# Kernel tuning notes

Measured on AMD Instinct MI355X. Metric: run time of the kernel, lower is better.

The kernel has to match this reference:

```python
import jax, jax.numpy as jnp
import numpy as np

LEAK = 0.01
EPS = 1e-5


def _gcn(x, W, b, src, dst, n):
    # GCNConv: add self-loops, symmetric D^-1/2 (A+I) D^-1/2 normalization
    h = x @ W
    loop = jnp.arange(n)
    s = jnp.concatenate([src, loop])
    d = jnp.concatenate([dst, loop])
    deg = jax.ops.segment_sum(jnp.ones(s.shape[0], h.dtype), d, num_segments=n)
    dinv = jnp.where(deg > 0, jax.lax.rsqrt(deg), 0.0)
    norm = dinv[s] * dinv[d]
    out = jax.ops.segment_sum(h[s] * norm[:, None], d, num_segments=n)
    return out + b


def _sage(x, Wl, bl, Wr, src, dst, n):
    # SAGEConv (mean aggr): lin_l(mean_neigh) + lin_r(x); bias on lin_l
    cnt = jax.ops.segment_sum(jnp.ones(src.shape[0], x.dtype), dst, num_segments=n)
    agg = jax.ops.segment_sum(x[src], dst, num_segments=n) / jnp.maximum(cnt, 1.0)[:, None]
    return agg @ Wl + bl + x @ Wr


def _bn(x, g, b):
    # BatchNorm over node dim, batch statistics (training forward), biased var
    m = x.mean(0)
    v = jnp.mean((x - m) ** 2, axis=0)
    return (x - m) * jax.lax.rsqrt(v + EPS) * g + b


def _lrelu(x):
    return jnp.where(x >= 0, x, LEAK * x)


def setup_inputs() -> dict:
    key = jax.random.key(0)
    ks = jax.random.split(key, 20)
    N, E, F_IN, H, G, L = 50000, 800000, 128, 128, 1000, 1000
    h2, h4, OUT = H // 2, H // 4, 32
    x = jax.random.normal(ks[0], (N, F_IN), dtype=jnp.float32)
    edge_index = jax.random.randint(ks[1], (2, E), 0, N)
    batch = jnp.sort(jax.random.randint(ks[2], (N,), 0, G))
    link_indices = jax.random.randint(ks[3], (2, L), 0, G)
    s = 0.05
    return {
        "x": x, "edge_index": edge_index, "batch": batch,
        "link_indices": link_indices, "num_graphs": G,
        "W1": jax.random.normal(ks[4], (F_IN, H), jnp.float32) * s,
        "b1": jnp.zeros((H,), jnp.float32),
        "g1": jnp.ones((H,), jnp.float32), "be1": jnp.zeros((H,), jnp.float32),
        "Wl2": jax.random.normal(ks[5], (H, h2), jnp.float32) * s,
        "bl2": jnp.zeros((h2,), jnp.float32),
        "Wr2": jax.random.normal(ks[6], (H, h2), jnp.float32) * s,
        "g2": jnp.ones((h2,), jnp.float32), "be2": jnp.zeros((h2,), jnp.float32),
        "W3": jax.random.normal(ks[7], (h2, h4), jnp.float32) * s,
        "b3": jnp.zeros((h4,), jnp.float32),
        "g3": jnp.ones((h4,), jnp.float32), "be3": jnp.zeros((h4,), jnp.float32),
        "W4": jax.random.normal(ks[8], (h4, OUT), jnp.float32) * s,
        "b4": jnp.zeros((OUT,), jnp.float32),
    }


def reference(x, edge_index, batch, link_indices, num_graphs,
              W1, b1, g1, be1, Wl2, bl2, Wr2, g2, be2,
              W3, b3, g3, be3, W4, b4):
    n = x.shape[0]
    src, dst = edge_index[0], edge_index[1]
    h = _lrelu(_bn(_gcn(x, W1, b1, src, dst, n), g1, be1))        # dropout = identity (eval)
    h = _lrelu(_bn(_sage(h, Wl2, bl2, Wr2, src, dst, n), g2, be2))
    h = _lrelu(_bn(_gcn(h, W3, b3, src, dst, n), g3, be3))
    h = _gcn(h, W4, b4, src, dst, n)
    g = jax.ops.segment_sum(h, batch, num_segments=num_graphs)     # global_add_pool
    src_emb = g[link_indices[0]]
    tgt_emb = g[link_indices[1]]
    return jax.nn.sigmoid(jnp.sum(src_emb * tgt_emb, axis=1))
```

## Files before the change

kernel.cpp:

```cpp
#include <hip/hip_runtime.h>
#include <math.h>

#define LEAK 0.01f
#define BNEPS 1e-5f
#define NCH 256
#define NGMAX 1024

typedef __attribute__((ext_vector_type(8))) short bf16x8;
typedef __attribute__((ext_vector_type(4))) float f32x4;
typedef __attribute__((ext_vector_type(2))) float f32x2;

__device__ inline unsigned bfpack(float a, float b) {
  unsigned ua = __float_as_uint(a);
  unsigned ub = __float_as_uint(b);
  unsigned ra = (ua + 0x7fffu + ((ua >> 16) & 1u)) >> 16;
  unsigned rb = (ub + 0x7fffu + ((ub >> 16) & 1u)) & 0xffff0000u;
  return ra | rb;
}
__device__ inline unsigned short bfround(float a) {
  unsigned ua = __float_as_uint(a);
  return (unsigned short)((ua + 0x7fffu + ((ua >> 16) & 1u)) >> 16);
}
__device__ inline float2 bfunpack(unsigned u) {
  float2 r;
  r.x = __uint_as_float(u << 16);
  r.y = __uint_as_float(u & 0xffff0000u);
  return r;
}
__device__ inline unsigned char f32_to_fp8(float v) {
  int p = __builtin_amdgcn_cvt_pk_fp8_f32(v, v, 0, false);
  return (unsigned char)(p & 0xff);
}

__global__ __launch_bounds__(256) void k_hist(const int* __restrict__ dst,
                                              int* __restrict__ H, int E, int NBK) {
  __shared__ int h[256];
  h[threadIdx.x] = 0;
  __syncthreads();
  int chunk = (E + NCH - 1) / NCH;
  int lo = blockIdx.x * chunk, hi = min(lo + chunk, E);
  for (int e = lo + threadIdx.x; e < hi; e += 256)
    atomicAdd(&h[dst[e] >> 8], 1);
  __syncthreads();
  if (threadIdx.x < NBK) H[threadIdx.x * NCH + blockIdx.x] = h[threadIdx.x];
}

__global__ __launch_bounds__(256) void k_gscan1(const int* __restrict__ in,
                                                int* __restrict__ bsum, int m) {
  int i = blockIdx.x * 256 + threadIdx.x;
  int v = (i < m) ? in[i] : 0;
#pragma unroll
  for (int s = 1; s < 64; s <<= 1) v += __shfl_xor(v, s, 64);
  __shared__ int ws[4];
  if ((threadIdx.x & 63) == 0) ws[threadIdx.x >> 6] = v;
  __syncthreads();
  if (threadIdx.x == 0) bsum[blockIdx.x] = ws[0] + ws[1] + ws[2] + ws[3];
}
__global__ __launch_bounds__(256) void k_gscan2(int* __restrict__ bsum, int NB) {
  __shared__ int lds[256];
  int t = threadIdx.x;
  int v = (t < NB) ? bsum[t] : 0;
  lds[t] = v;
  __syncthreads();
  for (int ofs = 1; ofs < 256; ofs <<= 1) {
    int u = (t >= ofs) ? lds[t - ofs] : 0;
    __syncthreads();
    lds[t] += u;
    __syncthreads();
  }
  if (t < NB) bsum[t] = lds[t] - v;
}
__global__ __launch_bounds__(256) void k_gscan3(const int* __restrict__ in,
                                                const int* __restrict__ boff,
                                                int* __restrict__ out, int m) {
  __shared__ int lds[256];
  int t = threadIdx.x;
  int i = blockIdx.x * 256 + t;
  int v = (i < m) ? in[i] : 0;
  lds[t] = v;
  __syncthreads();
  for (int ofs = 1; ofs < 256; ofs <<= 1) {
    int u = (t >= ofs) ? lds[t - ofs] : 0;
    __syncthreads();
    lds[t] += u;
    __syncthreads();
  }
  if (i < m) out[i] = boff[blockIdx.x] + lds[t] - v;
}

__global__ __launch_bounds__(256) void k_scatter_bkt(
    const int* __restrict__ src, const int* __restrict__ dst,
    const int* __restrict__ O, int* __restrict__ ebuf, int E, int NBK) {
  __shared__ int cur[256];
  if (threadIdx.x < NBK) cur[threadIdx.x] = O[threadIdx.x * NCH + blockIdx.x];
  __syncthreads();
  int chunk = (E + NCH - 1) / NCH;
  int lo = blockIdx.x * chunk, hi = min(lo + chunk, E);
  for (int e = lo + threadIdx.x; e < hi; e += 256) {
    int d = dst[e];
    int pos = atomicAdd(&cur[d >> 8], 1);
    ebuf[pos] = src[e] | ((d & 255) << 24);
  }
}

__global__ __launch_bounds__(256) void k_fill2(
    const int* __restrict__ ebuf, const int* __restrict__ O,
    int* __restrict__ eidx, int* __restrict__ rowptr,
    float* __restrict__ dinv, float* __restrict__ invcnt,
    int E, int n, int NBK) {
  __shared__ int hist[256];
  __shared__ int sc[256];
  __shared__ int cur[256];
  const int b = blockIdx.x;
  const int t = threadIdx.x;
  const int lo = O[b * NCH];
  const int hi = (b + 1 < NBK) ? O[(b + 1) * NCH] : E;
  hist[t] = 0;
  __syncthreads();
  for (int e = lo + t; e < hi; e += 256)
    atomicAdd(&hist[(ebuf[e] >> 24) & 255], 1);
  __syncthreads();
  int v = hist[t];
  sc[t] = v;
  __syncthreads();
  for (int ofs = 1; ofs < 256; ofs <<= 1) {
    int u = (t >= ofs) ? sc[t - ofs] : 0;
    __syncthreads();
    sc[t] += u;
    __syncthreads();
  }
  int excl = sc[t] - v;
  cur[t] = lo + excl;
  int node = b * 256 + t;
  if (node < n) {
    rowptr[node] = lo + excl;
    float d = (float)v;
    dinv[node]   = rsqrtf(d + 1.0f);
    invcnt[node] = 1.0f / fmaxf(d, 1.0f);
  }
  if (node == n || (b == NBK - 1 && t == 255)) rowptr[n] = E;
  __syncthreads();
  for (int e = lo + t; e < hi; e += 256) {
    int p = ebuf[e];
    int pos = atomicAdd(&cur[(p >> 24) & 255], 1);
    eidx[pos] = p & 0xFFFFFF;
  }
}

template<int F, bool GCN, bool OUTBF, bool ADD>
__global__ __launch_bounds__(256) void k_gather(
    const unsigned short* __restrict__ Hs, const float* __restrict__ scale,
    const int* __restrict__ rowptr, const int* __restrict__ eidx,
    const float* __restrict__ bias, const float* __restrict__ addf,
    float* __restrict__ outf, unsigned short* __restrict__ outb, int n) {
  constexpr int COLS = F / 8;
  constexpr int EPI  = 64 / COLS;
  const int v = blockIdx.x * 4 + (threadIdx.x >> 6);
  if (v >= n) return;
  const int lane = threadIdx.x & 63;
  const int col  = lane % COLS;
  const int eo   = lane / COLS;

  const int lo = rowptr[v], hi = rowptr[v + 1];
  float a[8] = {0.f,0.f,0.f,0.f,0.f,0.f,0.f,0.f};
  int myE = (lo + lane < hi) ? eidx[lo + lane] : 0;
  for (int base = lo; base < hi; base += 64) {
    int cnt = min(hi - base, 64);
    int nxt = (base + 64 + lane < hi) ? eidx[base + 64 + lane] : 0;
#pragma unroll 4
    for (int t = eo; t < cnt; t += EPI) {
      int s = __shfl(myE, t, 64);
      uint4 hv = *(const uint4*)&Hs[(long long)s * F + col * 8];
      float2 p0 = bfunpack(hv.x), p1 = bfunpack(hv.y);
      float2 p2 = bfunpack(hv.z), p3 = bfunpack(hv.w);
      a[0]+=p0.x; a[1]+=p0.y; a[2]+=p1.x; a[3]+=p1.y;
      a[4]+=p2.x; a[5]+=p2.y; a[6]+=p3.x; a[7]+=p3.y;
    }
    myE = nxt;
  }
#pragma unroll
  for (int m = COLS; m < 64; m <<= 1) {
#pragma unroll
    for (int j = 0; j < 8; j++) a[j] += __shfl_xor(a[j], m, 64);
  }
  if (eo == 0) {
    float sv = scale[v];
    float o[8];
    if constexpr (GCN) {
      uint4 hv = *(const uint4*)&Hs[(long long)v * F + col * 8];
      float2 p0 = bfunpack(hv.x), p1 = bfunpack(hv.y);
      float2 p2 = bfunpack(hv.z), p3 = bfunpack(hv.w);
      float h[8] = {p0.x,p0.y,p1.x,p1.y,p2.x,p2.y,p3.x,p3.y};
#pragma unroll
      for (int j = 0; j < 8; j++) o[j] = bias[col * 8 + j] + sv * (a[j] + h[j]);
    } else if constexpr (ADD) {
      const float4 t0 = *(const float4*)&addf[(long long)v * F + col * 8];
      const float4 t1 = *(const float4*)&addf[(long long)v * F + col * 8 + 4];
      o[0]=fmaf(sv,a[0],t0.x); o[1]=fmaf(sv,a[1],t0.y);
      o[2]=fmaf(sv,a[2],t0.z); o[3]=fmaf(sv,a[3],t0.w);
      o[4]=fmaf(sv,a[4],t1.x); o[5]=fmaf(sv,a[5],t1.y);
      o[6]=fmaf(sv,a[6],t1.z); o[7]=fmaf(sv,a[7],t1.w);
    } else {
#pragma unroll
      for (int j = 0; j < 8; j++) o[j] = sv * a[j];
    }
    if constexpr (OUTBF) {
      uint4 u;
      u.x = bfpack(o[0], o[1]); u.y = bfpack(o[2], o[3]);
      u.z = bfpack(o[4], o[5]); u.w = bfpack(o[6], o[7]);
      *(uint4*)&outb[(long long)v * F + col * 8] = u;
    } else {
      float4 o0 = {o[0],o[1],o[2],o[3]}, o1 = {o[4],o[5],o[6],o[7]};
      *(float4*)&outf[(long long)v * F + col * 8]     = o0;
      *(float4*)&outf[(long long)v * F + col * 8 + 4] = o1;
    }
  }
}

template<int F, bool GCN, bool ADD>
__global__ __launch_bounds__(256) void k_gather_fp8(
    const unsigned char* __restrict__ Hf8, const unsigned short* __restrict__ Hbf,
    const float* __restrict__ scale,
    const int* __restrict__ rowptr, const int* __restrict__ eidx,
    const float* __restrict__ bias, const float* __restrict__ addf,
    unsigned short* __restrict__ outb, int n) {
  constexpr int COLS = F / 8;
  constexpr int EPI  = 64 / COLS;
  const int v = blockIdx.x * 4 + (threadIdx.x >> 6);
  if (v >= n) return;
  const int lane = threadIdx.x & 63;
  const int col  = lane % COLS;
  const int eo   = lane / COLS;

  const int lo = rowptr[v], hi = rowptr[v + 1];
  float a[8] = {0.f,0.f,0.f,0.f,0.f,0.f,0.f,0.f};
  int myE = (lo + lane < hi) ? eidx[lo + lane] : 0;
  for (int base = lo; base < hi; base += 64) {
    int cnt = min(hi - base, 64);
    int nxt = (base + 64 + lane < hi) ? eidx[base + 64 + lane] : 0;
#pragma unroll 4
    for (int t = eo; t < cnt; t += EPI) {
      int s = __shfl(myE, t, 64);
      uint2 q = *(const uint2*)&Hf8[(long long)s * F + col * 8];
      f32x2 p0 = __builtin_amdgcn_cvt_pk_f32_fp8(q.x, false);
      f32x2 p1 = __builtin_amdgcn_cvt_pk_f32_fp8(q.x, true);
      f32x2 p2 = __builtin_amdgcn_cvt_pk_f32_fp8(q.y, false);
      f32x2 p3 = __builtin_amdgcn_cvt_pk_f32_fp8(q.y, true);
      a[0]+=p0[0]; a[1]+=p0[1]; a[2]+=p1[0]; a[3]+=p1[1];
      a[4]+=p2[0]; a[5]+=p2[1]; a[6]+=p3[0]; a[7]+=p3[1];
    }
    myE = nxt;
  }
#pragma unroll
  for (int m = COLS; m < 64; m <<= 1) {
#pragma unroll
    for (int j = 0; j < 8; j++) a[j] += __shfl_xor(a[j], m, 64);
  }
  if (eo == 0) {
    float sv = scale[v];
    float o[8];
    if constexpr (GCN) {
      uint4 hv = *(const uint4*)&Hbf[(long long)v * F + col * 8];
      float2 p0 = bfunpack(hv.x), p1 = bfunpack(hv.y);
      float2 p2 = bfunpack(hv.z), p3 = bfunpack(hv.w);
      float h[8] = {p0.x,p0.y,p1.x,p1.y,p2.x,p2.y,p3.x,p3.y};
#pragma unroll
      for (int j = 0; j < 8; j++) o[j] = bias[col * 8 + j] + sv * (a[j] + h[j]);
    } else if constexpr (ADD) {
      const float4 t0 = *(const float4*)&addf[(long long)v * F + col * 8];
      const float4 t1 = *(const float4*)&addf[(long long)v * F + col * 8 + 4];
      o[0]=fmaf(sv,a[0],t0.x); o[1]=fmaf(sv,a[1],t0.y);
      o[2]=fmaf(sv,a[2],t0.z); o[3]=fmaf(sv,a[3],t0.w);
      o[4]=fmaf(sv,a[4],t1.x); o[5]=fmaf(sv,a[5],t1.y);
      o[6]=fmaf(sv,a[6],t1.z); o[7]=fmaf(sv,a[7],t1.w);
    } else {
#pragma unroll
      for (int j = 0; j < 8; j++) o[j] = sv * a[j];
    }
    uint4 u;
    u.x = bfpack(o[0], o[1]); u.y = bfpack(o[2], o[3]);
    u.z = bfpack(o[4], o[5]); u.w = bfpack(o[6], o[7]);
    *(uint4*)&outb[(long long)v * F + col * 8] = u;
  }
}

template<int K, int F, bool XBF, bool BNIN, bool F8OUT>
__global__ __launch_bounds__(256) void k_gemm_mfma(
    const void* __restrict__ Xv, const float* __restrict__ W,
    const float* __restrict__ bnstats, const float* __restrict__ prescale,
    unsigned short* __restrict__ Yb, unsigned char* __restrict__ Yf8, int n) {
  constexpr int SP  = K + 8;
  constexpr int NCT = F / 16;
  __shared__ unsigned short sX[64 * SP];
  __shared__ unsigned short sWT[F * SP];
  __shared__ float sbn[BNIN ? 2 * K : 1];

  const int row0 = blockIdx.x * 64;
  if constexpr (BNIN) {
    for (int i = threadIdx.x; i < 2 * K; i += 256) sbn[i] = bnstats[i];
    __syncthreads();
  }
  for (int i = threadIdx.x; i < (K / 2) * F; i += 256) {
    int nn = i % F;
    int kk = (i / F) * 2;
    float w0 = W[(long long)kk * F + nn];
    float w1 = W[(long long)(kk + 1) * F + nn];
    *(unsigned*)&sWT[nn * SP + kk] = bfpack(w0, w1);
  }
  for (int i = threadIdx.x; i < 64 * (K / 8); i += 256) {
    int r = i / (K / 8), k8 = (i % (K / 8)) * 8;
    int gr = row0 + r;
    uint4 u = {0, 0, 0, 0};
    if (gr < n) {
      if constexpr (XBF) {
        const unsigned short* X = (const unsigned short*)Xv;
        uint4 raw = *(const uint4*)&X[(long long)gr * K + k8];
        if constexpr (BNIN) {
          float2 p0 = bfunpack(raw.x), p1 = bfunpack(raw.y);
          float2 p2 = bfunpack(raw.z), p3 = bfunpack(raw.w);
          float y[8] = {p0.x,p0.y,p1.x,p1.y,p2.x,p2.y,p3.x,p3.y};
#pragma unroll
          for (int j = 0; j < 8; j++) {
            float t = fmaf(y[j], sbn[k8 + j], sbn[K + k8 + j]);
            y[j] = (t >= 0.f) ? t : LEAK * t;
          }
          u.x = bfpack(y[0], y[1]); u.y = bfpack(y[2], y[3]);
          u.z = bfpack(y[4], y[5]); u.w = bfpack(y[6], y[7]);
        } else {
          u = raw;
        }
      } else {
        const float* X = (const float*)Xv;
        float4 xa = *(const float4*)&X[(long long)gr * K + k8];
        float4 xb = *(const float4*)&X[(long long)gr * K + k8 + 4];
        u.x = bfpack(xa.x, xa.y); u.y = bfpack(xa.z, xa.w);
        u.z = bfpack(xb.x, xb.y); u.w = bfpack(xb.z, xb.w);
      }
    }
    *(uint4*)&sX[r * SP + k8] = u;
  }
  __syncthreads();

  const int wv   = threadIdx.x >> 6;
  const int lane = threadIdx.x & 63;
  const int l16  = lane & 15;
  const int quad = lane >> 4;
  f32x4 acc[NCT];
#pragma unroll
  for (int c = 0; c < NCT; c++) acc[c] = (f32x4){0.f, 0.f, 0.f, 0.f};

#pragma unroll
  for (int k0 = 0; k0 < K; k0 += 32) {
    bf16x8 af = *(const bf16x8*)&sX[(wv * 16 + l16) * SP + k0 + quad * 8];
#pragma unroll
    for (int c = 0; c < NCT; c++) {
      bf16x8 bfr = *(const bf16x8*)&sWT[(c * 16 + l16) * SP + k0 + quad * 8];
      acc[c] = __builtin_amdgcn_mfma_f32_16x16x32_bf16(af, bfr, acc[c], 0, 0, 0);
    }
  }

  const int rbase = row0 + wv * 16 + quad * 4;
  float ps[4];
#pragma unroll
  for (int rg = 0; rg < 4; rg++) {
    int gr = rbase + rg;
    ps[rg] = (prescale && gr < n) ? prescale[gr] : 1.0f;
  }
#pragma unroll
  for (int c = 0; c < NCT; c++) {
    int col = c * 16 + l16;
#pragma unroll
    for (int rg = 0; rg < 4; rg++) {
      int gr = rbase + rg;
      if (gr < n) {
        float val = acc[c][rg] * ps[rg];
        Yb[(long long)gr * F + col] = bfround(val);
        if constexpr (F8OUT) Yf8[(long long)gr * F + col] = f32_to_fp8(val);
      }
    }
  }
}

__global__ __launch_bounds__(256) void k_gemm_sage_mfma(
    const unsigned short* __restrict__ X, const float* __restrict__ Wl,
    const float* __restrict__ Wr, const float* __restrict__ bl,
    const float* __restrict__ bnstats,
    unsigned char* __restrict__ t1f8, float* __restrict__ t2, int n) {
  constexpr int K = 128, F = 64, SP = K + 8, NCT = F / 16;
  __shared__ unsigned short sX[64 * SP];
  __shared__ unsigned short sWlT[F * SP];
  __shared__ unsigned short sWrT[F * SP];
  __shared__ float sbn[2 * K];

  for (int i = threadIdx.x; i < 2 * K; i += 256) sbn[i] = bnstats[i];
  __syncthreads();
  const int row0 = blockIdx.x * 64;
  for (int i = threadIdx.x; i < (K / 2) * F; i += 256) {
    int nn = i % F;
    int kk = (i / F) * 2;
    *(unsigned*)&sWlT[nn * SP + kk] =
        bfpack(Wl[(long long)kk * F + nn], Wl[(long long)(kk + 1) * F + nn]);
    *(unsigned*)&sWrT[nn * SP + kk] =
        bfpack(Wr[(long long)kk * F + nn], Wr[(long long)(kk + 1) * F + nn]);
  }
  for (int i = threadIdx.x; i < 64 * (K / 8); i += 256) {
    int r = i / (K / 8), k8 = (i % (K / 8)) * 8;
    int gr = row0 + r;
    uint4 u = {0, 0, 0, 0};
    if (gr < n) {
      uint4 raw = *(const uint4*)&X[(long long)gr * K + k8];
      float2 p0 = bfunpack(raw.x), p1 = bfunpack(raw.y);
      float2 p2 = bfunpack(raw.z), p3 = bfunpack(raw.w);
      float y[8] = {p0.x,p0.y,p1.x,p1.y,p2.x,p2.y,p3.x,p3.y};
#pragma unroll
      for (int j = 0; j < 8; j++) {
        float t = fmaf(y[j], sbn[k8 + j], sbn[K + k8 + j]);
        y[j] = (t >= 0.f) ? t : LEAK * t;
      }
      u.x = bfpack(y[0], y[1]); u.y = bfpack(y[2], y[3]);
      u.z = bfpack(y[4], y[5]); u.w = bfpack(y[6], y[7]);
    }
    *(uint4*)&sX[r * SP + k8] = u;
  }
  __syncthreads();

  const int wv   = threadIdx.x >> 6;
  const int lane = threadIdx.x & 63;
  const int l16  = lane & 15;
  const int quad = lane >> 4;
  f32x4 a1[NCT], a2[NCT];
#pragma unroll
  for (int c = 0; c < NCT; c++) {
    a1[c] = (f32x4){0.f, 0.f, 0.f, 0.f};
    a2[c] = (f32x4){0.f, 0.f, 0.f, 0.f};
  }
#pragma unroll
  for (int k0 = 0; k0 < K; k0 += 32) {
    bf16x8 af = *(const bf16x8*)&sX[(wv * 16 + l16) * SP + k0 + quad * 8];
#pragma unroll
    for (int c = 0; c < NCT; c++) {
      bf16x8 bl8 = *(const bf16x8*)&sWlT[(c * 16 + l16) * SP + k0 + quad * 8];
      bf16x8 br8 = *(const bf16x8*)&sWrT[(c * 16 + l16) * SP + k0 + quad * 8];
      a1[c] = __builtin_amdgcn_mfma_f32_16x16x32_bf16(af, bl8, a1[c], 0, 0, 0);
      a2[c] = __builtin_amdgcn_mfma_f32_16x16x32_bf16(af, br8, a2[c], 0, 0, 0);
    }
  }
  const int rbase = row0 + wv * 16 + quad * 4;
#pragma unroll
  for (int c = 0; c < NCT; c++) {
    int col = c * 16 + l16;
    float blv = bl[col];
#pragma unroll
    for (int rg = 0; rg < 4; rg++) {
      int gr = rbase + rg;
      if (gr < n) {
        t1f8[(long long)gr * F + col] = f32_to_fp8(a1[c][rg]);
        t2[(long long)gr * F + col]   = a2[c][rg] + blv;
      }
    }
  }
}

template<int F>
__global__ __launch_bounds__(256) void k_bn_stats(const unsigned short* __restrict__ Y,
                                                  float* __restrict__ partials, int n) {
  constexpr int FP  = F / 2;
  constexpr int RPB = 256 / FP;
  const int f2 = threadIdx.x % FP;
  const int r0 = threadIdx.x / FP;
  const unsigned* Yu = (const unsigned*)Y;
  float s1a = 0.f, s2a = 0.f, s1b = 0.f, s2b = 0.f;
  for (long long r = (long long)blockIdx.x * RPB + r0; r < n; r += 256LL * RPB) {
    float2 p = bfunpack(Yu[r * FP + f2]);
    s1a += p.x; s2a += p.x * p.x;
    s1b += p.y; s2b += p.y * p.y;
  }
  __shared__ float l1a[256], l2a[256], l1b[256], l2b[256];
  l1a[threadIdx.x] = s1a; l2a[threadIdx.x] = s2a;
  l1b[threadIdx.x] = s1b; l2b[threadIdx.x] = s2b;
  __syncthreads();
  if (r0 == 0) {
#pragma unroll
    for (int i = 1; i < RPB; i++) {
      s1a += l1a[i * FP + f2]; s2a += l2a[i * FP + f2];
      s1b += l1b[i * FP + f2]; s2b += l2b[i * FP + f2];
    }
    float* p = &partials[blockIdx.x * 2 * F];
    p[2 * f2]         = s1a;
    p[2 * f2 + 1]     = s1b;
    p[F + 2 * f2]     = s2a;
    p[F + 2 * f2 + 1] = s2b;
  }
}

__global__ void k_bn_finalize(const float* __restrict__ partials, float* __restrict__ stats,
                              const float* __restrict__ g, const float* __restrict__ be,
                              int F, float invN) {
  int f = threadIdx.x;
  if (f >= F) return;
  float s1 = 0.f, s2 = 0.f;
  for (int b = 0; b < 256; b++) {
    s1 += partials[b * 2 * F + f];
    s2 += partials[b * 2 * F + F + f];
  }
  float m   = s1 * invN;
  float var = s2 * invN - m * m;
  float sc  = g[f] * rsqrtf(var + BNEPS);
  stats[f]     = sc;
  stats[F + f] = be[f] - m * sc;
}

__global__ __launch_bounds__(256) void k_pool2(const float* __restrict__ a4,
                                               const int* __restrict__ batch,
                                               float* __restrict__ gpool, int n) {
  int g = blockIdx.x * 4 + (threadIdx.x >> 6);
  if (g >= NGMAX) return;
  int lane = threadIdx.x & 63;
  int s = 0, e = n;
  while (s < e) { int m = (s + e) >> 1; if (batch[m] < g) s = m + 1; else e = m; }
  int s2 = s, e2 = n;
  while (s2 < e2) { int m = (s2 + e2) >> 1; if (batch[m] < g + 1) s2 = m + 1; else e2 = m; }
  int f = lane & 31, ro = lane >> 5;
  float acc = 0.f;
  for (int r = s + ro; r < s2; r += 2) acc += a4[(long long)r * 32 + f];
  acc += __shfl_xor(acc, 32, 64);
  if (lane < 32) gpool[(long long)g * 32 + f] = acc;
}

__global__ void k_link(const float* __restrict__ g, const int* __restrict__ li0,
                       const int* __restrict__ li1, float* __restrict__ out, int L) {
  int i = blockIdx.x * blockDim.x + threadIdx.x;
  if (i >= L) return;
  const float* a = g + (long long)li0[i] * 32;
  const float* b = g + (long long)li1[i] * 32;
  float s = 0.f;
#pragma unroll
  for (int f = 0; f < 32; f++) s = fmaf(a[f], b[f], s);
  out[i] = 1.0f / (1.0f + expf(-s));
}

extern "C" void kernel_launch(void* const* d_in, const int* in_sizes, int n_in,
                              void* d_out, int out_size, void* d_ws, size_t ws_size,
                              hipStream_t stream) {
  const float* x   = (const float*)d_in[0];
  const int* ei    = (const int*)d_in[1];
  const int* batch = (const int*)d_in[2];
  const int* li    = (const int*)d_in[3];
  const float* W1  = (const float*)d_in[5];
  const float* b1  = (const float*)d_in[6];
  const float* g1  = (const float*)d_in[7];
  const float* be1 = (const float*)d_in[8];
  const float* Wl2 = (const float*)d_in[9];
  const float* bl2 = (const float*)d_in[10];
  const float* Wr2 = (const float*)d_in[11];
  const float* g2  = (const float*)d_in[12];
  const float* be2 = (const float*)d_in[13];
  const float* W3  = (const float*)d_in[14];
  const float* b3  = (const float*)d_in[15];
  const float* g3  = (const float*)d_in[16];
  const float* be3 = (const float*)d_in[17];
  const float* W4  = (const float*)d_in[18];
  const float* b4  = (const float*)d_in[19];

  const int n = in_sizes[0] / 128;
  const int E = in_sizes[1] / 2;
  const int L = in_sizes[3] / 2;
  const int* src = ei;
  const int* dst = ei + E;
  const int* li0 = li;
  const int* li1 = li + L;
  const int NBK = (n + 255) / 256;

  char* base = (char*)d_ws;
  size_t off = 0;
  auto alloc = [&](size_t bytes) -> void* {
    void* p = (void*)(base + off);
    off = (off + bytes + 255) & ~(size_t)255;
    return p;
  };
  int*   H      = (int*)alloc((size_t)NBK * NCH * 4);
  int*   O      = (int*)alloc((size_t)NBK * NCH * 4);
  int*   hsum   = (int*)alloc((size_t)1024 * 4);
  int*   ebuf   = (int*)alloc((size_t)E * 4);
  int*   eidx   = (int*)alloc((size_t)E * 4);
  int*   rowptr = (int*)alloc((size_t)(n + 1) * 4);
  float* dinv   = (float*)alloc((size_t)n * 4);
  float* invcnt = (float*)alloc((size_t)n * 4);
  float* stats1 = (float*)alloc(256 * 4);
  float* stats2 = (float*)alloc(128 * 4);
  float* stats3 = (float*)alloc(64 * 4);
  float* partials = (float*)alloc((size_t)256 * 256 * 4);
  float* gpool  = (float*)alloc((size_t)NGMAX * 32 * 4);
  unsigned short* h1b  = (unsigned short*)alloc((size_t)n * 128 * 2);
  unsigned char*  h1f8 = (unsigned char*)alloc((size_t)n * 128);
  unsigned short* a1b  = (unsigned short*)alloc((size_t)n * 128 * 2);
  unsigned char*  t1f8 = (unsigned char*)alloc((size_t)n * 64);
  float*          t2f  = (float*)alloc((size_t)n * 64 * 4);
  unsigned short* h2b  = (unsigned short*)alloc((size_t)n * 64 * 2);
  unsigned short* h3gb = (unsigned short*)alloc((size_t)n * 32 * 2);
  unsigned short* a3b  = (unsigned short*)alloc((size_t)n * 32 * 2);
  unsigned short* h4b  = (unsigned short*)alloc((size_t)n * 32 * 2);
  float*          a4f  = (float*)alloc((size_t)n * 32 * 4);
  (void)ws_size; (void)n_in; (void)out_size;

  const int BT = 256;
  auto cdiv = [](long long a, long long b) { return (int)((a + b - 1) / b); };
  const int GB  = cdiv(n, 4);
  const int GM  = cdiv(n, 64);
  const int MH  = NBK * NCH;
  const int NBH = cdiv(MH, 256);

  k_hist<<<NCH, 256, 0, stream>>>(dst, H, E, NBK);
  k_gscan1<<<NBH, 256, 0, stream>>>(H, hsum, MH);
  k_gscan2<<<1, 256, 0, stream>>>(hsum, NBH);
  k_gscan3<<<NBH, 256, 0, stream>>>(H, hsum, O, MH);
  k_scatter_bkt<<<NCH, 256, 0, stream>>>(src, dst, O, ebuf, E, NBK);
  k_fill2<<<NBK, 256, 0, stream>>>(ebuf, O, eidx, rowptr, dinv, invcnt, E, n, NBK);

  k_gemm_mfma<128,128,false,false,true><<<GM, 256, 0, stream>>>(
      x, W1, nullptr, dinv, h1b, h1f8, n);
  k_gather_fp8<128,true,false><<<GB, 256, 0, stream>>>(
      h1f8, h1b, dinv, rowptr, eidx, b1, nullptr, a1b, n);
  k_bn_stats<128><<<256, 256, 0, stream>>>(a1b, partials, n);
  k_bn_finalize<<<1, 128, 0, stream>>>(partials, stats1, g1, be1, 128, 1.0f / n);

  k_gemm_sage_mfma<<<GM, 256, 0, stream>>>(a1b, Wl2, Wr2, bl2, stats1, t1f8, t2f, n);
  k_gather_fp8<64,false,true><<<GB, 256, 0, stream>>>(
      t1f8, nullptr, invcnt, rowptr, eidx, nullptr, t2f, h2b, n);
  k_bn_stats<64><<<256, 256, 0, stream>>>(h2b, partials, n);
  k_bn_finalize<<<1, 64, 0, stream>>>(partials, stats2, g2, be2, 64, 1.0f / n);

  k_gemm_mfma<64,32,true,true,false><<<GM, 256, 0, stream>>>(
      h2b, W3, stats2, dinv, h3gb, nullptr, n);
  k_gather<32,true,true,false><<<GB, 256, 0, stream>>>(
      h3gb, dinv, rowptr, eidx, b3, nullptr, nullptr, a3b, n);
  k_bn_stats<32><<<256, 256, 0, stream>>>(a3b, partials, n);
  k_bn_finalize<<<1, 32, 0, stream>>>(partials, stats3, g3, be3, 32, 1.0f / n);

  k_gemm_mfma<32,32,true,true,false><<<GM, 256, 0, stream>>>(
      a3b, W4, stats3, dinv, h4b, nullptr, n);
  k_gather<32,true,false,false><<<GB, 256, 0, stream>>>(
      h4b, dinv, rowptr, eidx, b4, nullptr, a4f, nullptr, n);

  k_pool2<<<NGMAX / 4, 256, 0, stream>>>(a4f, batch, gpool, n);
  k_link<<<cdiv(L, BT), BT, 0, stream>>>(gpool, li0, li1, (float*)d_out, L);
}
```

Baseline: 379.3 us.

## Fuse scan, BN finalize and link kernels via last-block atomics; widen fp8 gather

Merges several small dependent kernels into their producers using a last-block-done atomic counter pattern: the two scan passes, each BN stats/finalize pair, and pool plus link scoring. This removes five kernel launches and their inter-kernel gaps. The fp8 gather also has each lane read 16 bytes instead of 8, so more edges are processed per lane step with fewer column lanes. The counters are zeroed in the first kernel, and the final reduction now runs in a single block after a threadfence, which adds atomics and serialized tail work.

After: 740.4 us. 95.2% more time.

```diff
diff --git a/kernel.cpp b/kernel.cpp
--- a/kernel.cpp
+++ b/kernel.cpp
@@ -33,7 +33,9 @@
 }
 
 __global__ __launch_bounds__(256) void k_hist(const int* __restrict__ dst,
-                                              int* __restrict__ H, int E, int NBK) {
+                                              int* __restrict__ H,
+                                              int* __restrict__ cnts, int E, int NBK) {
+  if (blockIdx.x == 0 && threadIdx.x < 8) cnts[threadIdx.x] = 0;
   __shared__ int h[256];
   h[threadIdx.x] = 0;
   __syncthreads();
@@ -45,22 +47,32 @@
   if (threadIdx.x < NBK) H[threadIdx.x * NCH + blockIdx.x] = h[threadIdx.x];
 }
 
-__global__ __launch_bounds__(256) void k_gscan1(const int* __restrict__ in,
-                                                int* __restrict__ bsum, int m) {
+__global__ __launch_bounds__(256) void k_gscan12(const int* __restrict__ in,
+                                                 int* __restrict__ bsum,
+                                                 int* __restrict__ boff,
+                                                 int* __restrict__ cnt, int m) {
   int i = blockIdx.x * 256 + threadIdx.x;
   int v = (i < m) ? in[i] : 0;
 #pragma unroll
   for (int s = 1; s < 64; s <<= 1) v += __shfl_xor(v, s, 64);
   __shared__ int ws[4];
+  __shared__ int done;
   if ((threadIdx.x & 63) == 0) ws[threadIdx.x >> 6] = v;
   __syncthreads();
-  if (threadIdx.x == 0) bsum[blockIdx.x] = ws[0] + ws[1] + ws[2] + ws[3];
-}
-__global__ __launch_bounds__(256) void k_gscan2(int* __restrict__ bsum, int NB) {
+  if (threadIdx.x == 0) {
+    bsum[blockIdx.x] = ws[0] + ws[1] + ws[2] + ws[3];
+    __threadfence();
+    done = atomicAdd(cnt, 1);
+  }
+  __syncthreads();
+  if (done != gridDim.x - 1) return;
+  __threadfence();
+  volatile int* vb = bsum;
+  int t = threadIdx.x;
+  int NB = gridDim.x;
   __shared__ int lds[256];
-  int t = threadIdx.x;
-  int v = (t < NB) ? bsum[t] : 0;
-  lds[t] = v;
+  int x = (t < NB) ? vb[t] : 0;
+  lds[t] = x;
   __syncthreads();
   for (int ofs = 1; ofs < 256; ofs <<= 1) {
     int u = (t >= ofs) ? lds[t - ofs] : 0;
@@ -68,8 +80,9 @@
     lds[t] += u;
     __syncthreads();
   }
-  if (t < NB) bsum[t] = lds[t] - v;
-}
+  if (t < NB) boff[t] = lds[t] - x;
+}
+
 __global__ __launch_bounds__(256) void k_gscan3(const int* __restrict__ in,
                                                 const int* __restrict__ boff,
                                                 int* __restrict__ out, int m) {
@@ -224,7 +237,7 @@
     const int* __restrict__ rowptr, const int* __restrict__ eidx,
     const float* __restrict__ bias, const float* __restrict__ addf,
     unsigned short* __restrict__ outb, int n) {
-  constexpr int COLS = F / 8;
+  constexpr int COLS = F / 16;
   constexpr int EPI  = 64 / COLS;
   const int v = blockIdx.x * 4 + (threadIdx.x >> 6);
   if (v >= n) return;
@@ -233,7 +246,9 @@
   const int eo   = lane / COLS;
 
   const int lo = rowptr[v], hi = rowptr[v + 1];
-  float a[8] = {0.f,0.f,0.f,0.f,0.f,0.f,0.f,0.f};
+  float a[16];
+#pragma unroll
+  for (int j = 0; j < 16; j++) a[j] = 0.f;
   int myE = (lo + lane < hi) ? eidx[lo + lane] : 0;
   for (int base = lo; base < hi; base += 64) {
     int cnt = min(hi - base, 64);
@@ -241,46 +256,54 @@
 #pragma unroll 4
     for (int t = eo; t < cnt; t += EPI) {
       int s = __shfl(myE, t, 64);
-      uint2 q = *(const uint2*)&Hf8[(long long)s * F + col * 8];
+      uint4 q = *(const uint4*)&Hf8[(long long)s * F + col * 16];
       f32x2 p0 = __builtin_amdgcn_cvt_pk_f32_fp8(q.x, false);
       f32x2 p1 = __builtin_amdgcn_cvt_pk_f32_fp8(q.x, true);
       f32x2 p2 = __builtin_amdgcn_cvt_pk_f32_fp8(q.y, false);
       f32x2 p3 = __builtin_amdgcn_cvt_pk_f32_fp8(q.y, true);
-      a[0]+=p0[0]; a[1]+=p0[1]; a[2]+=p1[0]; a[3]+=p1[1];
-      a[4]+=p2[0]; a[5]+=p2[1]; a[6]+=p3[0]; a[7]+=p3[1];
+      f32x2 p4 = __builtin_amdgcn_cvt_pk_f32_fp8(q.z, false);
+      f32x2 p5 = __builtin_amdgcn_cvt_pk_f32_fp8(q.z, true);
+      f32x2 p6 = __builtin_amdgcn_cvt_pk_f32_fp8(q.w, false);
+      f32x2 p7 = __builtin_amdgcn_cvt_pk_f32_fp8(q.w, true);
+      a[0]+=p0[0];  a[1]+=p0[1];  a[2]+=p1[0];  a[3]+=p1[1];
+      a[4]+=p2[0];  a[5]+=p2[1];  a[6]+=p3[0];  a[7]+=p3[1];
+      a[8]+=p4[0];  a[9]+=p4[1];  a[10]+=p5[0]; a[11]+=p5[1];
+      a[12]+=p6[0]; a[13]+=p6[1]; a[14]+=p7[0]; a[15]+=p7[1];
     }
     myE = nxt;
   }
 #pragma unroll
   for (int m = COLS; m < 64; m <<= 1) {
 #pragma unroll
-    for (int j = 0; j < 8; j++) a[j] += __shfl_xor(a[j], m, 64);
+    for (int j = 0; j < 16; j++) a[j] += __shfl_xor(a[j], m, 64);
   }
   if (eo == 0) {
     float sv = scale[v];
-    float o[8];
+    float o[16];
     if constexpr (GCN) {
-      uint4 hv = *(const uint4*)&Hbf[(long long)v * F + col * 8];
-      float2 p0 = bfunpack(hv.x), p1 = bfunpack(hv.y);
-      float2 p2 = bfunpack(hv.z), p3 = bfunpack(hv.w);
-      float h[8] = {p0.x,p0.y,p1.x,p1.y,p2.x,p2.y,p3.x,p3.y};
-#pragma unroll
-      for (int j = 0; j < 8; j++) o[j] = bias[col * 8 + j] + sv * (a[j] + h[j]);
+      uint4 h0 = *(const uint4*)&Hbf[(long long)v * F + col * 16];
+      uint4 h1 = *(const uint4*)&Hbf[(long long)v * F + col * 16 + 8];
+      float2 q0 = bfunpack(h0.x), q1 = bfunpack(h0.y), q2 = bfunpack(h0.z), q3 = bfunpack(h0.w);
+      float2 q4 = bfunpack(h1.x), q5 = bfunpack(h1.y), q6 = bfunpack(h1.z), q7 = bfunpack(h1.w);
+      float h[16] = {q0.x,q0.y,q1.x,q1.y,q2.x,q2.y,q3.x,q3.y,
+                     q4.x,q4.y,q5.x,q5.y,q6.x,q6.y,q7.x,q7.y};
+#pragma unroll
+      for (int j = 0; j < 16; j++) o[j] = bias[col * 16 + j] + sv * (a[j] + h[j]);
     } else if constexpr (ADD) {
-      const float4 t0 = *(const float4*)&addf[(long long)v * F + col * 8];
-      const float4 t1 = *(const float4*)&addf[(long long)v * F + col * 8 + 4];
-      o[0]=fmaf(sv,a[0],t0.x); o[1]=fmaf(sv,a[1],t0.y);
-      o[2]=fmaf(sv,a[2],t0.z); o[3]=fmaf(sv,a[3],t0.w);
-      o[4]=fmaf(sv,a[4],t1.x); o[5]=fmaf(sv,a[5],t1.y);
-      o[6]=fmaf(sv,a[6],t1.z); o[7]=fmaf(sv,a[7],t1.w);
+      const float* ap = &addf[(long long)v * F + col * 16];
+#pragma unroll
+      for (int j = 0; j < 16; j++) o[j] = fmaf(sv, a[j], ap[j]);
     } else {
 #pragma unroll
-      for (int j = 0; j < 8; j++) o[j] = sv * a[j];
-    }
-    uint4 u;
-    u.x = bfpack(o[0], o[1]); u.y = bfpack(o[2], o[3]);
-    u.z = bfpack(o[4], o[5]); u.w = bfpack(o[6], o[7]);
-    *(uint4*)&outb[(long long)v * F + col * 8] = u;
+      for (int j = 0; j < 16; j++) o[j] = sv * a[j];
+    }
+    uint4 u0, u1;
+    u0.x = bfpack(o[0],o[1]);   u0.y = bfpack(o[2],o[3]);
+    u0.z = bfpack(o[4],o[5]);   u0.w = bfpack(o[6],o[7]);
+    u1.x = bfpack(o[8],o[9]);   u1.y = bfpack(o[10],o[11]);
+    u1.z = bfpack(o[12],o[13]); u1.w = bfpack(o[14],o[15]);
+    *(uint4*)&outb[(long long)v * F + col * 16]     = u0;
+    *(uint4*)&outb[(long long)v * F + col * 16 + 8] = u1;
   }
 }
 
@@ -462,8 +485,10 @@
 }
 
 template<int F>
-__global__ __launch_bounds__(256) void k_bn_stats(const unsigned short* __restrict__ Y,
-                                                  float* __restrict__ partials, int n) {
+__global__ __launch_bounds__(256) void k_bn_stats(
+    const unsigned short* __restrict__ Y, float* __restrict__ partials,
+    const float* __restrict__ g, const float* __restrict__ be,
+    float* __restrict__ stats, float invN, int* __restrict__ cnt, int n) {
   constexpr int FP  = F / 2;
   constexpr int RPB = 256 / FP;
   const int f2 = threadIdx.x % FP;
@@ -476,6 +501,7 @@
     s1b += p.y; s2b += p.y * p.y;
   }
   __shared__ float l1a[256], l2a[256], l1b[256], l2b[256];
+  __shared__ int done;
   l1a[threadIdx.x] = s1a; l2a[threadIdx.x] = s2a;
   l1b[threadIdx.x] = s1b; l2b[threadIdx.x] = s2b;
   __syncthreads();
@@ -491,17 +517,21 @@
     p[F + 2 * f2]     = s2a;
     p[F + 2 * f2 + 1] = s2b;
   }
-}
-
-__global__ void k_bn_finalize(const float* __restrict__ partials, float* __restrict__ stats,
-                              const float* __restrict__ g, const float* __restrict__ be,
-                              int F, float invN) {
+  __syncthreads();
+  if (threadIdx.x == 0) {
+    __threadfence();
+    done = atomicAdd(cnt, 1);
+  }
+  __syncthreads();
+  if (done != gridDim.x - 1) return;
+  __threadfence();
+  volatile float* vp = partials;
   int f = threadIdx.x;
   if (f >= F) return;
   float s1 = 0.f, s2 = 0.f;
   for (int b = 0; b < 256; b++) {
-    s1 += partials[b * 2 * F + f];
-    s2 += partials[b * 2 * F + F + f];
+    s1 += vp[b * 2 * F + f];
+    s2 += vp[b * 2 * F + F + f];
   }
   float m   = s1 * invN;
   float var = s2 * invN - m * m;
@@ -510,33 +540,42 @@
   stats[F + f] = be[f] - m * sc;
 }
 
-__global__ __launch_bounds__(256) void k_pool2(const float* __restrict__ a4,
-                                               const int* __restrict__ batch,
-                                               float* __restrict__ gpool, int n) {
+__global__ __launch_bounds__(256) void k_pool_link(
+    const float* __restrict__ a4, const int* __restrict__ batch,
+    float* __restrict__ gpool, const int* __restrict__ li0,
+    const int* __restrict__ li1, float* __restrict__ out,
+    int* __restrict__ cnt, int n, int L) {
   int g = blockIdx.x * 4 + (threadIdx.x >> 6);
-  if (g >= NGMAX) return;
   int lane = threadIdx.x & 63;
-  int s = 0, e = n;
-  while (s < e) { int m = (s + e) >> 1; if (batch[m] < g) s = m + 1; else e = m; }
-  int s2 = s, e2 = n;
-  while (s2 < e2) { int m = (s2 + e2) >> 1; if (batch[m] < g + 1) s2 = m + 1; else e2 = m; }
-  int f = lane & 31, ro = lane >> 5;
-  float acc = 0.f;
-  for (int r = s + ro; r < s2; r += 2) acc += a4[(long long)r * 32 + f];
-  acc += __shfl_xor(acc, 32, 64);
-  if (lane < 32) gpool[(long long)g * 32 + f] = acc;
-}
-
-__global__ void k_link(const float* __restrict__ g, const int* __restrict__ li0,
-                       const int* __restrict__ li1, float* __restrict__ out, int L) {
-  int i = blockIdx.x * blockDim.x + threadIdx.x;
-  if (i >= L) return;
-  const float* a = g + (long long)li0[i] * 32;
-  const float* b = g + (long long)li1[i] * 32;
-  float s = 0.f;
-#pragma unroll
-  for (int f = 0; f < 32; f++) s = fmaf(a[f], b[f], s);
-  out[i] = 1.0f / (1.0f + expf(-s));
+  if (g < NGMAX) {
+    int s = 0, e = n;
+    while (s < e) { int m = (s + e) >> 1; if (batch[m] < g) s = m + 1; else e = m; }
+    int s2 = s, e2 = n;
+    while (s2 < e2) { int m = (s2 + e2) >> 1; if (batch[m] < g + 1) s2 = m + 1; else e2 = m; }
+    int f = lane & 31, ro = lane >> 5;
+    float acc = 0.f;
+    for (int r = s + ro; r < s2; r += 2) acc += a4[(long long)r * 32 + f];
+    acc += __shfl_xor(acc, 32, 64);
+    if (lane < 32) gpool[(long long)g * 32 + f] = acc;
+  }
+  __shared__ int done;
+  __syncthreads();
+  if (threadIdx.x == 0) {
+    __threadfence();
+    done = atomicAdd(cnt, 1);
+  }
+  __syncthreads();
+  if (done != gridDim.x - 1) return;
+  __threadfence();
+  volatile float* vg = gpool;
+  for (int i = threadIdx.x; i < L; i += 256) {
+    const volatile float* a = vg + (long long)li0[i] * 32;
+    const volatile float* b = vg + (long long)li1[i] * 32;
+    float s = 0.f;
+#pragma unroll
+    for (int f = 0; f < 32; f++) s = fmaf(a[f], b[f], s);
+    out[i] = 1.0f / (1.0f + expf(-s));
+  }
 }
 
 extern "C" void kernel_launch(void* const* d_in, const int* in_sizes, int n_in,
@@ -578,9 +617,11 @@
     off = (off + bytes + 255) & ~(size_t)255;
     return p;
   };
+  int*   cnts   = (int*)alloc(8 * 4);
   int*   H      = (int*)alloc((size_t)NBK * NCH * 4);
   int*   O      = (int*)alloc((size_t)NBK * NCH * 4);
-  int*   hsum   = (int*)alloc((size_t)1024 * 4);
+  int*   bsum   = (int*)alloc((size_t)1024 * 4);
+  int*   boff   = (int*)alloc((size_t)1024 * 4);
   int*   ebuf   = (int*)alloc((size_t)E * 4);
   int*   eidx   = (int*)alloc((size_t)E * 4);
   int*   rowptr = (int*)alloc((size_t)(n + 1) * 4);
@@ -603,17 +644,15 @@
   float*          a4f  = (float*)alloc((size_t)n * 32 * 4);
   (void)ws_size; (void)n_in; (void)out_size;
 
-  const int BT = 256;
   auto cdiv = [](long long a, long long b) { return (int)((a + b - 1) / b); };
   const int GB  = cdiv(n, 4);
   const int GM  = cdiv(n, 64);
   const int MH  = NBK * NCH;
   const int NBH = cdiv(MH, 256);
 
-  k_hist<<<NCH, 256, 0, stream>>>(dst, H, E, NBK);
-  k_gscan1<<<NBH, 256, 0, stream>>>(H, hsum, MH);
-  k_gscan2<<<1, 256, 0, stream>>>(hsum, NBH);
-  k_gscan3<<<NBH, 256, 0, stream>>>(H, hsum, O, MH);
+  k_hist<<<NCH, 256, 0, stream>>>(dst, H, cnts, E, NBK);
+  k_gscan12<<<NBH, 256, 0, stream>>>(H, bsum, boff, &cnts[0], MH);
+  k_gscan3<<<NBH, 256, 0, stream>>>(H, boff, O, MH);
   k_scatter_bkt<<<NCH, 256, 0, stream>>>(src, dst, O, ebuf, E, NBK);
   k_fill2<<<NBK, 256, 0, stream>>>(ebuf, O, eidx, rowptr, dinv, invcnt, E, n, NBK);
 
@@ -621,27 +660,27 @@
       x, W1, nullptr, dinv, h1b, h1f8, n);
   k_gather_fp8<128,true,false><<<GB, 256, 0, stream>>>(
       h1f8, h1b, dinv, rowptr, eidx, b1, nullptr, a1b, n);
-  k_bn_stats<128><<<256, 256, 0, stream>>>(a1b, partials, n);
-  k_bn_finalize<<<1, 128, 0, stream>>>(partials, stats1, g1, be1, 128, 1.0f / n);
+  k_bn_stats<128><<<256, 256, 0, stream>>>(a1b, partials, g1, be1, stats1,
+                                           1.0f / n, &cnts[1], n);
 
   k_gemm_sage_mfma<<<GM, 256, 0, stream>>>(a1b, Wl2, Wr2, bl2, stats1, t1f8, t2f, n);
   k_gather_fp8<64,false,true><<<GB, 256, 0, stream>>>(
       t1f8, nullptr, invcnt, rowptr, eidx, nullptr, t2f, h2b, n);
-  k_bn_stats<64><<<256, 256, 0, stream>>>(h2b, partials, n);
-  k_bn_finalize<<<1, 64, 0, stream>>>(partials, stats2, g2, be2, 64, 1.0f / n);
+  k_bn_stats<64><<<256, 256, 0, stream>>>(h2b, partials, g2, be2, stats2,
+                                          1.0f / n, &cnts[2], n);
 
   k_gemm_mfma<64,32,true,true,false><<<GM, 256, 0, stream>>>(
       h2b, W3, stats2, dinv, h3gb, nullptr, n);
   k_gather<32,true,true,false><<<GB, 256, 0, stream>>>(
       h3gb, dinv, rowptr, eidx, b3, nullptr, nullptr, a3b, n);
-  k_bn_stats<32><<<256, 256, 0, stream>>>(a3b, partials, n);
-  k_bn_finalize<<<1, 32, 0, stream>>>(partials, stats3, g3, be3, 32, 1.0f / n);
+  k_bn_stats<32><<<256, 256, 0, stream>>>(a3b, partials, g3, be3, stats3,
+                                          1.0f / n, &cnts[3], n);
 
   k_gemm_mfma<32,32,true,true,false><<<GM, 256, 0, stream>>>(
       a3b, W4, stats3, dinv, h4b, nullptr, n);
   k_gather<32,true,false,false><<<GB, 256, 0, stream>>>(
       h4b, dinv, rowptr, eidx, b4, nullptr, a4f, nullptr, n);
 
-  k_pool2<<<NGMAX / 4, 256, 0, stream>>>(a4f, batch, gpool, n);
-  k_link<<<cdiv(L, BT), BT, 0, stream>>>(gpool, li0, li1, (float*)d_out, L);
-}
+  k_pool_link<<<NGMAX / 4, 256, 0, stream>>>(a4f, batch, gpool, li0, li1,
+                                             (float*)d_out, &cnts[4], n, L);
+}
```
